# Kernel optimization log

Hardware: AMD Instinct MI355X
Metric: run time of the kernel (lower is better)

The kernel has to match this reference:

```python
import jax, jax.numpy as jnp
from jax import lax
import numpy as np

B, S, E, H2, V = 128, 256, 256, 256, 50000  # batch, subword seq len, emb dim, per-direction hidden, vocab


def _make_masks(rng):
    # random subword lengths, word-start (bmask) and word-end (fmask) masks with equal counts per row
    lengths = rng.integers(S // 2, S + 1, size=B)
    pos = np.arange(S)[None, :]
    valid = pos < lengths[:, None]
    starts = (rng.random((B, S)) < 0.33) & valid
    starts[:, 0] = True
    nxt = np.concatenate([starts[:, 1:], np.zeros((B, 1), bool)], axis=1)
    fmask = valid & (nxt | (pos == lengths[:, None] - 1))
    return valid, fmask, starts


def setup_inputs():
    rng = np.random.default_rng(0)
    valid, fmask, bmask = _make_masks(rng)
    sw_ids = rng.integers(1, V, size=(B, S)) * valid  # 0 = pad
    key = jax.random.key(0)
    ks = jax.random.split(key, 8)
    se = float(np.sqrt(3.0 / E))       # random_embedding scale
    sh = float(1.0 / np.sqrt(H2))      # pytorch LSTM init scale
    u = lambda k, shape, s: jax.random.uniform(k, shape, jnp.float32, -s, s)
    return {
        "sw_ids": jnp.asarray(sw_ids, jnp.int32),
        "fmasks": jnp.asarray(fmask, jnp.int32),
        "bmasks": jnp.asarray(bmask, jnp.int32),
        "emb_W": u(ks[0], (V, E), se),
        "W_ih_f": u(ks[1], (4 * H2, E), sh),
        "W_hh_f": u(ks[2], (4 * H2, H2), sh),
        "b_f": u(ks[3], (4 * H2,), sh),
        "W_ih_b": u(ks[4], (4 * H2, E), sh),
        "W_hh_b": u(ks[5], (4 * H2, H2), sh),
        "b_b": u(ks[6], (4 * H2,), sh),
    }


def _lstm(x, mask, Wih, Whh, b):
    # x: [B,S,E]; mask: [B,S] float. Matches packed LSTM: state frozen and output
    # zeroed at padded steps (pad_packed_sequence zero-pads). Gate order i,f,g,o.
    h0 = jnp.zeros((x.shape[0], Whh.shape[1]), x.dtype)

    def step(carry, inp):
        h, c = carry
        xt, mt = inp
        g = xt @ Wih.T + h @ Whh.T + b
        i, f, gg, o = jnp.split(g, 4, axis=-1)
        c_new = jax.nn.sigmoid(f) * c + jax.nn.sigmoid(i) * jnp.tanh(gg)
        h_new = jax.nn.sigmoid(o) * jnp.tanh(c_new)
        m = mt[:, None]
        h = jnp.where(m > 0, h_new, h)
        c = jnp.where(m > 0, c_new, c)
        return (h, c), h * m

    _, ys = lax.scan(step, (h0, h0), (x.transpose(1, 0, 2), mask.T))
    return ys.transpose(1, 0, 2)  # [B,S,H2]


def _select_pad(out, mask, out_len):
    # vectorized masked_select + pad_sequence: stable-sort moves mask==1 positions
    # (in original order) to the front of the time axis, then zero beyond out_len.
    gather = jnp.argsort(1 - mask, axis=1)  # stable -> selected positions first
    sel = jnp.take_along_axis(out, gather[:, :, None], axis=1)
    word_valid = jnp.arange(out.shape[1])[None, :] < out_len[:, None]
    return sel * word_valid[:, :, None].astype(out.dtype)


def reference(sw_ids, fmasks, bmasks, emb_W, W_ih_f, W_hh_f, b_f, W_ih_b, W_hh_b, b_b):
    lengths = (sw_ids != 0).sum(axis=1)
    perm = jnp.argsort(-lengths)  # stable descending, like torch sort(descending=True)
    ids = sw_ids[perm]
    fm = fmasks[perm]
    bm = bmasks[perm]
    valid = (ids != 0).astype(emb_W.dtype)
    embeds = emb_W[ids]  # dropout is identity at eval time
    f_out = _lstm(embeds, valid, W_ih_f, W_hh_f, b_f)
    # backward direction: reverse in time (padding leads but state stays zero under mask)
    b_out = _lstm(embeds[:, ::-1], valid[:, ::-1], W_ih_b, W_hh_b, b_b)[:, ::-1]
    out_len = fm.sum(axis=1)
    f_pad = _select_pad(f_out, fm, out_len)
    b_pad = _select_pad(b_out, bm, out_len)
    perm2 = jnp.argsort(-out_len)
    out = jnp.concatenate([f_pad[perm2], b_pad[perm2]], axis=2)  # [B, S, 2*H2]
    return out, out_len[perm2]
```

## Files before the change

### kernel.cpp

```cpp
#include <hip/hip_runtime.h>
#include <hip/hip_bf16.h>
#include <hip/hip_fp16.h>
#include <math.h>
#include <stdint.h>

#define BB 128
#define SS 256
#define EE 256
#define HH 256
#define G4 1024
#define OUT_HEAD (BB*SS*2*HH)
#define SE 0.10825317547305482f

#define P8_HH_F 0
#define P8_HH_B 65536
#define P8_IH_F 131072
#define P8_IH_B 196608
#define SC_OFF  (1024*1024)
#define INT_OFF (1280*1024)
#define GX_OFF  (4*1024*1024)

__device__ __forceinline__ float sigf(float x){ return 1.0f/(1.0f+__expf(-x)); }
__device__ __forceinline__ float tanhx(float x){
    float t = __expf(2.0f*x);
    return 1.0f - 2.0f/(t+1.0f);
}
__device__ __forceinline__ int dot4(uint32_t a, uint32_t b, int acc){
    return __builtin_amdgcn_sdot4((int)a, (int)b, acc, false);
}

__global__ __launch_bounds__(64) void pack8(const float* __restrict__ W,
    uint32_t* __restrict__ P8, float* __restrict__ SC){
    const int g = blockIdx.x, lane = threadIdx.x;
    float4 w4 = ((const float4*)(W + (size_t)g*EE))[lane];
    float m = fmaxf(fmaxf(fabsf(w4.x), fabsf(w4.y)), fmaxf(fabsf(w4.z), fabsf(w4.w)));
    for(int off=32; off; off>>=1) m = fmaxf(m, __shfl_xor(m, off));
    const float inv = (m > 0.f) ? 127.f/m : 0.f;
    int b0 = (int)rintf(w4.x*inv), b1 = (int)rintf(w4.y*inv);
    int b2 = (int)rintf(w4.z*inv), b3 = (int)rintf(w4.w*inv);
    uint32_t p = (uint32_t)(b0 & 0xff) | ((uint32_t)(b1 & 0xff) << 8) |
                 ((uint32_t)(b2 & 0xff) << 16) | ((uint32_t)(b3 & 0xff) << 24);
    P8[lane*G4 + g] = p;
    if(lane == 0) SC[g] = m / 127.f;
}

__global__ void prep(const int* __restrict__ sw, const int* __restrict__ fm,
                     const int* __restrict__ bm, int* __restrict__ wsI,
                     float* __restrict__ out_tail){
    __shared__ int len_s[BB], flen_s[BB], perm_s[BB], olp_s[BB];
    int b = threadIdx.x;
    int cnt = 0, fcnt = 0;
    for(int t=0;t<SS;t++){
        cnt  += (sw[b*SS+t] != 0);
        fcnt += fm[b*SS+t];
    }
    len_s[b] = cnt; flen_s[b] = fcnt;
    __syncthreads();
    int r = 0;
    for(int b2=0;b2<BB;b2++){
        int l2 = len_s[b2];
        r += (l2 > cnt) || (l2 == cnt && b2 < b);
    }
    perm_s[r] = b;
    __syncthreads();
    int orig = perm_s[b];
    olp_s[b] = flen_s[orig];
    wsI[0*BB + b] = orig;
    wsI[1*BB + b] = len_s[orig];
    __syncthreads();
    int v = olp_s[b];
    int q = 0;
    for(int r2=0;r2<BB;r2++){
        int v2 = olp_s[r2];
        q += (v2 > v) || (v2 == v && r2 < b);
    }
    wsI[2*BB + b] = q;
    wsI[3*BB + b] = v;
    out_tail[q] = (float)v;
    int* fdst = wsI + 4*BB;
    int* bdst = fdst + BB*SS;
    int fc = 0, bc = 0;
    for(int t=0;t<SS;t++){
        int fv = fm[orig*SS+t];
        fdst[b*SS+t] = (fv && fc < v) ? (q*SS + fc) : -1;
        fc += fv;
        int bv = bm[orig*SS+t];
        bdst[b*SS+t] = (bv && bc < v) ? (q*SS + bc) : -1;
        bc += bv;
    }
}

__global__ __launch_bounds__(1024,4) void xg8(const int* __restrict__ sw,
    const float* __restrict__ emb, const float* __restrict__ b_f,
    const float* __restrict__ b_b, const uint32_t* __restrict__ wsU,
    const float* __restrict__ scl, const int* __restrict__ wsI,
    _Float16* __restrict__ gx){
    __shared__ int x8i[64];
    const int tid = threadIdx.x, r = blockIdx.x, dir = blockIdx.y;
    const uint32_t* P = wsU + (dir ? P8_IH_B : P8_IH_F);
    uint32_t w[64];
    #pragma unroll
    for(int j=0;j<64;j++) w[j] = P[j*G4 + tid];
    const float cs = scl[(2 + dir)*G4 + tid] * (SE/127.f);
    const float bias = (dir ? b_b : b_f)[tid];
    const int orig = wsI[r], L = wsI[BB + r];
    const int* ids = sw + orig*SS;
    float xv = 0.f;
    if(tid < EE) xv = emb[(size_t)ids[0]*EE + tid];
    _Float16* gxr = gx + ((size_t)(dir*BB + r))*SS*G4;

    for(int t=0;t<L;t++){
        if(tid < EE) ((signed char*)x8i)[tid] = (signed char)(int)rintf(xv*(127.f/SE));
        __syncthreads();
        if(tid < EE && t+1 < L) xv = emb[(size_t)ids[t+1]*EE + tid];
        int acc0 = 0, acc1 = 0;
        const uint4* hp = (const uint4*)x8i;
        #pragma unroll
        for(int j=0;j<16;j++){
            uint4 hv = hp[j];
            acc0 = dot4(w[4*j+0], hv.x, acc0);
            acc1 = dot4(w[4*j+1], hv.y, acc1);
            acc0 = dot4(w[4*j+2], hv.z, acc0);
            acc1 = dot4(w[4*j+3], hv.w, acc1);
        }
        gxr[(size_t)t*G4 + tid] = (_Float16)(bias + (float)(acc0 + acc1)*cs);
        __syncthreads();
    }
}

__global__ __launch_bounds__(1024,4) void rec8(const uint32_t* __restrict__ wsU,
    const float* __restrict__ scl, const int* __restrict__ wsI,
    const _Float16* __restrict__ gx, float* __restrict__ out){
    __shared__ int h8i[64];
    __shared__ float gfl[G4];
    const int tid = threadIdx.x, r = blockIdx.x, dir = blockIdx.y;
    const uint32_t* P = wsU + (dir ? P8_HH_B : P8_HH_F);
    uint32_t w[64];
    #pragma unroll
    for(int j=0;j<64;j++) w[j] = P[j*G4 + tid];
    const float csh = scl[dir*G4 + tid] * (1.f/127.f);
    const int L = wsI[BB + r];
    const int* dstA = wsI + 4*BB + (dir ? BB*SS : 0) + r*SS;
    if(tid < 64) h8i[tid] = 0;
    float cst = 0.f;
    const _Float16* gxr = gx + ((size_t)(dir*BB + r))*SS*G4;
    const int t0 = dir ? L-1 : 0, stp = dir ? -1 : 1;
    _Float16 gv = gxr[(size_t)t0*G4 + tid];
    __syncthreads();

    for(int s=0;s<L;s++){
        const int t = t0 + s*stp;
        const float gxv = (float)gv;
        if(s+1 < L) gv = gxr[(size_t)(t+stp)*G4 + tid];
        int acc0 = 0, acc1 = 0;
        const uint4* hp = (const uint4*)h8i;
        #pragma unroll
        for(int j=0;j<16;j++){
            uint4 hv = hp[j];
            acc0 = dot4(w[4*j+0], hv.x, acc0);
            acc1 = dot4(w[4*j+1], hv.y, acc1);
            acc0 = dot4(w[4*j+2], hv.z, acc0);
            acc1 = dot4(w[4*j+3], hv.w, acc1);
        }
        gfl[tid] = gxv + (float)(acc0 + acc1)*csh;
        __syncthreads();
        if(tid < HH){
            float gi = gfl[tid], gf = gfl[tid+256], gz = gfl[tid+512], go = gfl[tid+768];
            float i = sigf(gi), f = sigf(gf), z = tanhx(gz), o = sigf(go);
            cst = f*cst + i*z;
            float hn = o*tanhx(cst);
            ((signed char*)h8i)[tid] = (signed char)(int)rintf(hn*127.f);
            int dst = dstA[t];
            if(dst >= 0) out[(size_t)dst*(2*HH) + dir*HH + tid] = hn;
        }
        __syncthreads();
    }
}

extern "C" void kernel_launch(void* const* d_in, const int* in_sizes, int n_in,
                              void* d_out, int out_size, void* d_ws, size_t ws_size,
                              hipStream_t stream){
    const int*   sw    = (const int*)d_in[0];
    const int*   fm    = (const int*)d_in[1];
    const int*   bm    = (const int*)d_in[2];
    const float* emb   = (const float*)d_in[3];
    const float* Wih_f = (const float*)d_in[4];
    const float* Whh_f = (const float*)d_in[5];
    const float* b_f   = (const float*)d_in[6];
    const float* Wih_b = (const float*)d_in[7];
    const float* Whh_b = (const float*)d_in[8];
    const float* b_b   = (const float*)d_in[9];
    float* out = (float*)d_out;
    uint32_t* wsU = (uint32_t*)d_ws;
    float* scl = (float*)((char*)d_ws + SC_OFF);
    int* wsI = (int*)((char*)d_ws + INT_OFF);
    _Float16* gxp = (_Float16*)((char*)d_ws + GX_OFF);

    hipMemsetAsync(d_out, 0, (size_t)out_size*4, stream);
    pack8<<<G4, 64, 0, stream>>>(Whh_f, wsU + P8_HH_F, scl + 0*G4);
    pack8<<<G4, 64, 0, stream>>>(Whh_b, wsU + P8_HH_B, scl + 1*G4);
    pack8<<<G4, 64, 0, stream>>>(Wih_f, wsU + P8_IH_F, scl + 2*G4);
    pack8<<<G4, 64, 0, stream>>>(Wih_b, wsU + P8_IH_B, scl + 3*G4);
    prep<<<1, BB, 0, stream>>>(sw, fm, bm, wsI, out + OUT_HEAD);
    xg8<<<dim3(BB,2), 1024, 0, stream>>>(sw, emb, b_f, b_b, wsU, scl, wsI, gxp);
    rec8<<<dim3(BB,2), 1024, 0, stream>>>(wsU, scl, wsI, gxp, out);
}
```

Measured before the change: 523.6 us.

## Tile input-gate projection over 16 timesteps and vector-load recurrent weights

The input-gate kernel now processes 16 timesteps per block iteration. It quantizes 16 embedding rows into shared memory at once and streams the int8 weights from global memory, reusing each loaded weight across 16 accumulators. This replaces holding all weights in registers and synchronizing twice per timestep. The recurrent kernel switches to a gate-major weight layout and loads its 64 packed weights with 16 inline-asm dwordx4 loads pinned in registers, which keeps them resident and cuts the number of setup loads. The cost is extra global/L2 weight traffic per tile in the input kernel, more accumulator registers, and reliance on inline assembly.

```diff
diff --git a/kernel.cpp b/kernel.cpp
--- a/kernel.cpp
+++ b/kernel.cpp
@@ -20,6 +20,8 @@
 #define INT_OFF (1280*1024)
 #define GX_OFF  (4*1024*1024)
 
+typedef uint32_t u32x4 __attribute__((ext_vector_type(4)));
+
 __device__ __forceinline__ float sigf(float x){ return 1.0f/(1.0f+__expf(-x)); }
 __device__ __forceinline__ float tanhx(float x){
     float t = __expf(2.0f*x);
@@ -30,7 +32,7 @@
 }
 
 __global__ __launch_bounds__(64) void pack8(const float* __restrict__ W,
-    uint32_t* __restrict__ P8, float* __restrict__ SC){
+    uint32_t* __restrict__ P8, float* __restrict__ SC, int gmajor){
     const int g = blockIdx.x, lane = threadIdx.x;
     float4 w4 = ((const float4*)(W + (size_t)g*EE))[lane];
     float m = fmaxf(fmaxf(fabsf(w4.x), fabsf(w4.y)), fmaxf(fabsf(w4.z), fabsf(w4.w)));
@@ -40,7 +42,8 @@
     int b2 = (int)rintf(w4.z*inv), b3 = (int)rintf(w4.w*inv);
     uint32_t p = (uint32_t)(b0 & 0xff) | ((uint32_t)(b1 & 0xff) << 8) |
                  ((uint32_t)(b2 & 0xff) << 16) | ((uint32_t)(b3 & 0xff) << 24);
-    P8[lane*G4 + g] = p;
+    if(gmajor) P8[g*64 + lane] = p;
+    else       P8[lane*G4 + g] = p;
     if(lane == 0) SC[g] = m / 127.f;
 }
 
@@ -90,43 +93,59 @@
     }
 }
 
-__global__ __launch_bounds__(1024,4) void xg8(const int* __restrict__ sw,
+#define XDOT(k) { uint4 hv = xv[(k)*16 + j]; \
+    a##k = dot4(w0, hv.x, a##k); a##k = dot4(w1, hv.y, a##k); \
+    a##k = dot4(w2, hv.z, a##k); a##k = dot4(w3, hv.w, a##k); }
+#define XST(k) if(t0 + (k) < L) gxr[(size_t)(t0+(k))*G4 + tid] = (_Float16)(bias + (float)a##k*cs);
+
+__global__ __launch_bounds__(1024,4) void xg8t(const int* __restrict__ sw,
     const float* __restrict__ emb, const float* __restrict__ b_f,
     const float* __restrict__ b_b, const uint32_t* __restrict__ wsU,
     const float* __restrict__ scl, const int* __restrict__ wsI,
     _Float16* __restrict__ gx){
-    __shared__ int x8i[64];
+    __shared__ uint32_t xq[16*64];
     const int tid = threadIdx.x, r = blockIdx.x, dir = blockIdx.y;
     const uint32_t* P = wsU + (dir ? P8_IH_B : P8_IH_F);
-    uint32_t w[64];
-    #pragma unroll
-    for(int j=0;j<64;j++) w[j] = P[j*G4 + tid];
     const float cs = scl[(2 + dir)*G4 + tid] * (SE/127.f);
     const float bias = (dir ? b_b : b_f)[tid];
     const int orig = wsI[r], L = wsI[BB + r];
     const int* ids = sw + orig*SS;
-    float xv = 0.f;
-    if(tid < EE) xv = emb[(size_t)ids[0]*EE + tid];
     _Float16* gxr = gx + ((size_t)(dir*BB + r))*SS*G4;
-
-    for(int t=0;t<L;t++){
-        if(tid < EE) ((signed char*)x8i)[tid] = (signed char)(int)rintf(xv*(127.f/SE));
-        __syncthreads();
-        if(tid < EE && t+1 < L) xv = emb[(size_t)ids[t+1]*EE + tid];
-        int acc0 = 0, acc1 = 0;
-        const uint4* hp = (const uint4*)x8i;
-        #pragma unroll
+    const int k = tid >> 6;
+    const int e4 = (tid & 63);
+
+    for(int t0 = 0; t0 < L; t0 += 16){
+        int t = t0 + k;
+        float4 xf = ((const float4*)(emb + (size_t)ids[t]*EE))[e4];
+        int b0 = (int)rintf(xf.x*(127.f/SE)), b1 = (int)rintf(xf.y*(127.f/SE));
+        int b2 = (int)rintf(xf.z*(127.f/SE)), b3 = (int)rintf(xf.w*(127.f/SE));
+        xq[k*64 + e4] = (uint32_t)(b0 & 0xff) | ((uint32_t)(b1 & 0xff) << 8) |
+                        ((uint32_t)(b2 & 0xff) << 16) | ((uint32_t)(b3 & 0xff) << 24);
+        __syncthreads();
+        int a0=0,a1=0,a2=0,a3=0,a4=0,a5=0,a6=0,a7=0;
+        int a8=0,a9=0,a10=0,a11=0,a12=0,a13=0,a14=0,a15=0;
+        const uint4* xv = (const uint4*)xq;
         for(int j=0;j<16;j++){
-            uint4 hv = hp[j];
-            acc0 = dot4(w[4*j+0], hv.x, acc0);
-            acc1 = dot4(w[4*j+1], hv.y, acc1);
-            acc0 = dot4(w[4*j+2], hv.z, acc0);
-            acc1 = dot4(w[4*j+3], hv.w, acc1);
+            uint32_t w0 = P[(4*j+0)*G4 + tid];
+            uint32_t w1 = P[(4*j+1)*G4 + tid];
+            uint32_t w2 = P[(4*j+2)*G4 + tid];
+            uint32_t w3 = P[(4*j+3)*G4 + tid];
+            XDOT(0) XDOT(1) XDOT(2) XDOT(3) XDOT(4) XDOT(5) XDOT(6) XDOT(7)
+            XDOT(8) XDOT(9) XDOT(10) XDOT(11) XDOT(12) XDOT(13) XDOT(14) XDOT(15)
         }
-        gxr[(size_t)t*G4 + tid] = (_Float16)(bias + (float)(acc0 + acc1)*cs);
-        __syncthreads();
-    }
-}
+        XST(0) XST(1) XST(2) XST(3) XST(4) XST(5) XST(6) XST(7)
+        XST(8) XST(9) XST(10) XST(11) XST(12) XST(13) XST(14) XST(15)
+        __syncthreads();
+    }
+}
+
+#define LDQ(name, o) u32x4 name; \
+    asm volatile("global_load_dwordx4 %0, %1, off offset:" #o \
+                 : "=v"(name) : "v"(bptr) : "memory");
+#define PIN(name) asm volatile("" : "+v"(name));
+#define DOTQ(q, hvv) { uint4 hv = hvv; \
+    acc0 = dot4(q.x, hv.x, acc0); acc1 = dot4(q.y, hv.y, acc1); \
+    acc0 = dot4(q.z, hv.z, acc0); acc1 = dot4(q.w, hv.w, acc1); }
 
 __global__ __launch_bounds__(1024,4) void rec8(const uint32_t* __restrict__ wsU,
     const float* __restrict__ scl, const int* __restrict__ wsI,
@@ -134,10 +153,15 @@
     __shared__ int h8i[64];
     __shared__ float gfl[G4];
     const int tid = threadIdx.x, r = blockIdx.x, dir = blockIdx.y;
-    const uint32_t* P = wsU + (dir ? P8_HH_B : P8_HH_F);
-    uint32_t w[64];
-    #pragma unroll
-    for(int j=0;j<64;j++) w[j] = P[j*G4 + tid];
+    const uint32_t* bptr = wsU + (dir ? P8_HH_B : P8_HH_F) + (size_t)tid*64;
+    LDQ(q0,0)    LDQ(q1,16)   LDQ(q2,32)   LDQ(q3,48)
+    LDQ(q4,64)   LDQ(q5,80)   LDQ(q6,96)   LDQ(q7,112)
+    LDQ(q8,128)  LDQ(q9,144)  LDQ(q10,160) LDQ(q11,176)
+    LDQ(q12,192) LDQ(q13,208) LDQ(q14,224) LDQ(q15,240)
+    asm volatile("s_waitcnt vmcnt(0)" ::: "memory");
+    __builtin_amdgcn_sched_barrier(0);
+    PIN(q0) PIN(q1) PIN(q2) PIN(q3) PIN(q4) PIN(q5) PIN(q6) PIN(q7)
+    PIN(q8) PIN(q9) PIN(q10) PIN(q11) PIN(q12) PIN(q13) PIN(q14) PIN(q15)
     const float csh = scl[dir*G4 + tid] * (1.f/127.f);
     const int L = wsI[BB + r];
     const int* dstA = wsI + 4*BB + (dir ? BB*SS : 0) + r*SS;
@@ -154,14 +178,10 @@
         if(s+1 < L) gv = gxr[(size_t)(t+stp)*G4 + tid];
         int acc0 = 0, acc1 = 0;
         const uint4* hp = (const uint4*)h8i;
-        #pragma unroll
-        for(int j=0;j<16;j++){
-            uint4 hv = hp[j];
-            acc0 = dot4(w[4*j+0], hv.x, acc0);
-            acc1 = dot4(w[4*j+1], hv.y, acc1);
-            acc0 = dot4(w[4*j+2], hv.z, acc0);
-            acc1 = dot4(w[4*j+3], hv.w, acc1);
-        }
+        DOTQ(q0,  hp[0])  DOTQ(q1,  hp[1])  DOTQ(q2,  hp[2])  DOTQ(q3,  hp[3])
+        DOTQ(q4,  hp[4])  DOTQ(q5,  hp[5])  DOTQ(q6,  hp[6])  DOTQ(q7,  hp[7])
+        DOTQ(q8,  hp[8])  DOTQ(q9,  hp[9])  DOTQ(q10, hp[10]) DOTQ(q11, hp[11])
+        DOTQ(q12, hp[12]) DOTQ(q13, hp[13]) DOTQ(q14, hp[14]) DOTQ(q15, hp[15])
         gfl[tid] = gxv + (float)(acc0 + acc1)*csh;
         __syncthreads();
         if(tid < HH){
@@ -197,11 +217,11 @@
     _Float16* gxp = (_Float16*)((char*)d_ws + GX_OFF);
 
     hipMemsetAsync(d_out, 0, (size_t)out_size*4, stream);
-    pack8<<<G4, 64, 0, stream>>>(Whh_f, wsU + P8_HH_F, scl + 0*G4);
-    pack8<<<G4, 64, 0, stream>>>(Whh_b, wsU + P8_HH_B, scl + 1*G4);
-    pack8<<<G4, 64, 0, stream>>>(Wih_f, wsU + P8_IH_F, scl + 2*G4);
-    pack8<<<G4, 64, 0, stream>>>(Wih_b, wsU + P8_IH_B, scl + 3*G4);
+    pack8<<<G4, 64, 0, stream>>>(Whh_f, wsU + P8_HH_F, scl + 0*G4, 1);
+    pack8<<<G4, 64, 0, stream>>>(Whh_b, wsU + P8_HH_B, scl + 1*G4, 1);
+    pack8<<<G4, 64, 0, stream>>>(Wih_f, wsU + P8_IH_F, scl + 2*G4, 0);
+    pack8<<<G4, 64, 0, stream>>>(Wih_b, wsU + P8_IH_B, scl + 3*G4, 0);
     prep<<<1, BB, 0, stream>>>(sw, fm, bm, wsI, out + OUT_HEAD);
-    xg8<<<dim3(BB,2), 1024, 0, stream>>>(sw, emb, b_f, b_b, wsU, scl, wsI, gxp);
+    xg8t<<<dim3(BB,2), 1024, 0, stream>>>(sw, emb, b_f, b_b, wsU, scl, wsI, gxp);
     rec8<<<dim3(BB,2), 1024, 0, stream>>>(wsU, scl, wsI, gxp, out);
 }
```

Measured after the change: 519.5 us. No clear change (-0.8%).
